# Performance work log

Hardware: AMD Instinct MI355X
Metric: run time of the kernel (lower is better)

Reference implementation:

```python
import jax, jax.numpy as jnp
import numpy as np

NUM_GROUPS = 16
GN_EPS = 1e-5
POOL = 4
CLAMP_MIN, CLAMP_MAX = 0.0, 1.0


def setup_inputs() -> dict:
    key = jax.random.key(0)
    k = jax.random.split(key, 4)
    x = jax.random.normal(k[0], (128, 8, 128, 128), dtype=jnp.float32)
    conv_weight = jax.random.normal(k[1], (64, 8, 3, 3), dtype=jnp.float32) * 0.1
    conv_bias = jax.random.normal(k[2], (64,), dtype=jnp.float32) * 0.1
    gn_weight = jnp.ones((64,), dtype=jnp.float32)
    gn_bias = jnp.zeros((64,), dtype=jnp.float32)
    scale = jax.random.normal(k[3], (64, 1, 1), dtype=jnp.float32)
    return {"x": x, "conv_weight": conv_weight, "conv_bias": conv_bias,
            "gn_weight": gn_weight, "gn_bias": gn_bias, "scale": scale}


def reference(x, conv_weight, conv_bias, gn_weight, gn_bias, scale):
    # Conv2d 3x3, stride 1, padding 0 (torch defaults). NCHW / OIHW.
    y = jax.lax.conv_general_dilated(
        x, conv_weight, window_strides=(1, 1), padding='VALID',
        dimension_numbers=('NCHW', 'OIHW', 'NCHW'))
    y = y + conv_bias[None, :, None, None]  # [N, 64, 126, 126]

    # GroupNorm(16 groups over 64 channels): stats over (C//G, H, W) per group.
    N, C, H, W = y.shape
    g = y.reshape(N, NUM_GROUPS, C // NUM_GROUPS, H, W)
    mean = jnp.mean(g, axis=(2, 3, 4), keepdims=True)
    var = jnp.mean(jnp.square(g - mean), axis=(2, 3, 4), keepdims=True)
    g = (g - mean) * jax.lax.rsqrt(var + GN_EPS)
    y = g.reshape(N, C, H, W) * gn_weight[None, :, None, None] + gn_bias[None, :, None, None]

    # Per-channel scale (scale has shape [64, 1, 1], broadcasts over H, W).
    y = y * scale[None]

    # MaxPool2d(kernel=4, stride=4), floor mode -> 126 // 4 = 31.
    y = jax.lax.reduce_window(
        y, -jnp.inf, jax.lax.max,
        window_dimensions=(1, 1, POOL, POOL),
        window_strides=(1, 1, POOL, POOL), padding='VALID')

    # Clamp.
    return jnp.clip(y, CLAMP_MIN, CLAMP_MAX)
```

## Files before the change

### kernel.cpp

```cpp
#include <hip/hip_runtime.h>
#include <hip/hip_fp16.h>

namespace {
constexpr int ICH = 8, IH = 128, IW = 128;
constexpr int CPG = 4, PH = 31;
constexpr int ICS = 516;
constexpr float EPS = 1e-5f;
constexpr float MPX = 126.f * 126.f;
constexpr int TOTAL_OUT = 128 * 64 * PH * PH;
constexpr size_t XH_BYTES = (size_t)128 * 128 * 128 * 8 * 2;
constexpr size_t WS_NEED = XH_BYTES + (size_t)128 * 16 * 4 * 2 * 4;

typedef _Float16 v8h __attribute__((ext_vector_type(8)));
typedef float v4f __attribute__((ext_vector_type(4)));
typedef unsigned short u16;
typedef unsigned int u32;

__device__ __forceinline__ void gll16(const void* g, void* l) {
  __builtin_amdgcn_global_load_lds((const __attribute__((address_space(1))) void*)g,
                                   (__attribute__((address_space(3))) void*)l, 16, 0, 0);
}

__device__ __forceinline__ u32 pkh(float a, float b) {
  unsigned short lo = __half_as_ushort(__float2half_rn(a));
  unsigned short hi = __half_as_ushort(__float2half_rn(b));
  return (u32)lo | ((u32)hi << 16);
}

__global__ __launch_bounds__(256) void pack_f16x8(const float* __restrict__ x,
                                                  u16* __restrict__ xh) {
  int i = blockIdx.x * 256 + threadIdx.x;
  int n = i >> 14, rc = i & 16383;
  const float* bp = x + ((size_t)n << 17) + rc;
  uint4 o;
  o.x = pkh(bp[0],      bp[16384]);
  o.y = pkh(bp[32768],  bp[49152]);
  o.z = pkh(bp[65536],  bp[81920]);
  o.w = pkh(bp[98304],  bp[114688]);
  *reinterpret_cast<uint4*>(xh + (size_t)i * 8) = o;
}

__global__ __launch_bounds__(256, 2) void conv_mfma(
    const u16* __restrict__ xh, const float* __restrict__ cw,
    const float* __restrict__ cb, const float* __restrict__ gnw,
    const float* __restrict__ sc, float* __restrict__ out,
    float* __restrict__ wsp) {
  __shared__ __align__(16) u16 ring[12][1056];

  const int bid = blockIdx.x;
  const int n = bid >> 2, qq = bid & 3;
  const int out_lo = qq * 32;
  const int out_hi = (qq == 3) ? 125 : out_lo + 31;
  const int NST = (qq == 3) ? 8 : 9;
  const int t = threadIdx.x;
  const int w = t >> 6, l = t & 63;
  const int colB = l & 15, qt = l >> 4;

  for (int idx = t; idx < 12 * 32; idx += 256)
    ring[idx >> 5][1024 + (idx & 31)] = 0;

  v8h af[3];
#pragma unroll
  for (int kc = 0; kc < 3; ++kc) {
    const int tap = kc * 4 + qt;
    const int ocA = 16 * w + colB;
#pragma unroll
    for (int i = 0; i < 8; ++i)
      af[kc][i] = (tap < 9) ? (_Float16)cw[ocA * 72 + i * 9 + tap] : (_Float16)0.f;
  }
  int eofc[3], dhl[3];
#pragma unroll
  for (int kc = 0; kc < 3; ++kc) {
    int tap = kc * 4 + qt; tap = (tap > 8) ? 8 : tap;
    dhl[kc] = tap / 3;
    eofc[kc] = (colB + tap % 3) * 8;
  }
  float flip[4];
#pragma unroll
  for (int q = 0; q < 4; ++q) {
    int oc = 16 * w + qt * 4 + q;
    flip[q] = (gnw[oc] * sc[oc] >= 0.f) ? 1.f : -1.f;
  }
  const u16* rb = &ring[0][0];

  auto issue = [&](int s) {
#pragma unroll
    for (int k = 0; k < 2; ++k) {
      int mk = w * 2 + k;
      int grow = out_lo + 4 * s + (mk >> 1);
      int hv = mk & 1;
      int slot = grow % 12;
      gll16(xh + ((size_t)(n * 128 + grow) * 128 + hv * 64) * 8 + l * 8,
            (void*)&ring[slot][hv * 512]);
    }
  };

  issue(0);

  float s1q[4] = {0.f, 0.f, 0.f, 0.f};
  float s2g = 0.f;
  float pacc[8][4];
#pragma unroll
  for (int ci = 0; ci < 8; ++ci)
#pragma unroll
    for (int q = 0; q < 4; ++q) pacc[ci][q] = -3.4e38f;

  for (int s = 0; s < NST; ++s) {
    __syncthreads();
    if (s + 1 < NST) issue(s + 1);
#pragma unroll
    for (int ri = 0; ri < 4; ++ri) {
      const int r = out_lo + 4 * s - 2 + ri;
      if (r < out_lo || r > out_hi) continue;
      const int rm = r % 12;
      int eoff[3];
#pragma unroll
      for (int kc = 0; kc < 3; ++kc) {
        int sl = rm + dhl[kc];
        if (sl >= 12) sl -= 12;
        eoff[kc] = sl * 1056 + eofc[kc];
      }
#pragma unroll
      for (int ci = 0; ci < 8; ++ci) {
        v4f acc = {0.f, 0.f, 0.f, 0.f};
#pragma unroll
        for (int kc = 0; kc < 3; ++kc) {
          v8h bf = *reinterpret_cast<const v8h*>(rb + eoff[kc] + ci * 128);
          acc = __builtin_amdgcn_mfma_f32_16x16x32_f16(af[kc], bf, acc, 0, 0, 0);
        }
        if (ci < 7) {
#pragma unroll
          for (int q = 0; q < 4; ++q) {
            s1q[q] += acc[q];
            s2g = fmaf(acc[q], acc[q], s2g);
            pacc[ci][q] = fmaxf(pacc[ci][q], flip[q] * acc[q]);
          }
        } else {
          const bool va = (colB < 14);
#pragma unroll
          for (int q = 0; q < 4; ++q) {
            float a = va ? acc[q] : 0.f;
            s1q[q] += a;
            s2g = fmaf(a, a, s2g);
            float fv = va ? flip[q] * acc[q] : -3.4e38f;
            pacc[7][q] = fmaxf(pacc[7][q], fv);
          }
        }
      }
      if ((r & 3) == 3) {
        const int pr = r >> 2;
        float* ob = out + (((size_t)n * 64 + 16 * w + qt * 4) * PH + pr) * PH;
#pragma unroll
        for (int ci = 0; ci < 8; ++ci) {
#pragma unroll
          for (int q = 0; q < 4; ++q) {
            float pm = pacc[ci][q];
            pm = fmaxf(pm, __shfl_xor(pm, 1, 64));
            pm = fmaxf(pm, __shfl_xor(pm, 2, 64));
            if ((l & 3) == 0 && (ci < 7 || colB < 12)) {
              int pc = ci * 4 + (colB >> 2);
              ob[(size_t)q * (PH * PH) + pc] = flip[q] * pm;
            }
            pacc[ci][q] = -3.4e38f;
          }
        }
      }
    }
  }

#pragma unroll
  for (int off = 1; off <= 8; off <<= 1) {
#pragma unroll
    for (int q = 0; q < 4; ++q) s1q[q] += __shfl_xor(s1q[q], off, 64);
    s2g += __shfl_xor(s2g, off, 64);
  }
  if ((l & 15) == 0) {
    const float cntq = 126.f * (float)(out_hi - out_lo + 1);
    float S1 = 0.f, S2 = s2g;
#pragma unroll
    for (int q = 0; q < 4; ++q) {
      float b = cb[16 * w + qt * 4 + q];
      S1 += s1q[q] + cntq * b;
      S2 += 2.f * b * s1q[q] + cntq * b * b;
    }
    int g = 4 * w + qt;
    float* wp = wsp + ((size_t)(n * 16 + g) * 4 + qq) * 2;
    wp[0] = S1; wp[1] = S2;
  }
}

__global__ __launch_bounds__(256) void gn_affine_clamp(
    float* __restrict__ out, const float* __restrict__ wsp,
    const float* __restrict__ gnw, const float* __restrict__ gnb,
    const float* __restrict__ sc, const float* __restrict__ cb) {
  int i = blockIdx.x * 256 + threadIdx.x;
  const int stride = gridDim.x * 256;
  for (; i < TOTAL_OUT; i += stride) {
    int c = (i / 961) & 63;
    int n = i / 61504;
    const float* wp = wsp + ((size_t)(n * 16 + (c >> 2)) * 4) * 2;
    float S1 = wp[0] + wp[2] + wp[4] + wp[6];
    float S2 = wp[1] + wp[3] + wp[5] + wp[7];
    constexpr float invN = 1.f / (4.f * MPX);
    float mean = S1 * invN;
    float var = S2 * invN - mean * mean;
    float inv = rsqrtf(var + EPS);
    float gw = gnw[c];
    float A = gw * inv * sc[c];
    float B = (gnb[c] - mean * inv * gw) * sc[c] + A * cb[c];
    float v = fmaf(A, out[i], B);
    out[i] = fminf(fmaxf(v, 0.f), 1.f);
  }
}

#define FIN(T, DOSTATS, RE)                                                    \
  {                                                                            \
    float f0 = T[0] + __shfl_xor(T[0], 32, 64);                                \
    float f1 = T[1] + __shfl_xor(T[1], 32, 64);                                \
    float f2 = T[2] + __shfl_xor(T[2], 32, 64);                                \
    float f3 = T[3] + __shfl_xor(T[3], 32, 64);                                \
    if (DOSTATS) {                                                             \
      s1 += f0 + f1 + m23 * (f2 + f3);                                         \
      float qa = fmaf(f0, f0, f1 * f1);                                        \
      float qb = fmaf(f2, f2, f3 * f3);                                        \
      s2 += qa + m23 * qb;                                                     \
    }                                                                          \
    RE = fmaxf(fmaxf(flip * f0, flip * f1), fmaxf(flip * f2, flip * f3));      \
  }
#define ZERO(T) { T[0] = 0.f; T[1] = 0.f; T[2] = 0.f; T[3] = 0.f; }
#define ROWF(RR, T2, T1, T0)                                                   \
  {                                                                            \
    _Pragma("unroll") for (int i4 = 0; i4 < 4; ++i4) {                         \
      const float* rp = bp + (4 * p + i4) * ICS + (RR) * IW + 4 * j;           \
      float4 v4 = *reinterpret_cast<const float4*>(rp);                        \
      float2 v2 = *reinterpret_cast<const float2*>(rp + 4);                    \
      float in[6] = {v4.x, v4.y, v4.z, v4.w, v2.x, v2.y};                      \
      _Pragma("unroll") for (int dw = 0; dw < 3; ++dw) {                       \
        const float w0 = wf[i4 * 9 + dw];                                      \
        const float w1 = wf[i4 * 9 + 3 + dw];                                  \
        const float w2 = wf[i4 * 9 + 6 + dw];                                  \
        _Pragma("unroll") for (int q = 0; q < 4; ++q) {                        \
          T2[q] = fmaf(in[q + dw], w2, T2[q]);                                 \
          T1[q] = fmaf(in[q + dw], w1, T1[q]);                                 \
          T0[q] = fmaf(in[q + dw], w0, T0[q]);                                 \
        }                                                                      \
      }                                                                        \
    }                                                                          \
  }
#define STAGEF(S, X, Y, Z, DOS01, DOWIN)                                       \
  {                                                                            \
    __syncthreads();                                                           \
    const int cur = (S) & 1;                                                   \
    if ((S) < 31) issue(4 * ((S) + 1), cur ^ 1);                               \
    const float* bp = &buf[cur][0][0];                                         \
    float re0, re1, re2, re3;                                                  \
    ROWF(0, X, Y, Z) FIN(X, DOS01, re0) ZERO(X)                                \
    ROWF(1, Y, Z, X) FIN(Y, DOS01, re1) ZERO(Y)                                \
    if (DOWIN) {                                                               \
      float wfin = fmaxf(wprev, fmaxf(re0, re1));                              \
      if (p == 0 && j < 31) mm[c][(S) - 1][j] = __float2half(flip * wfin);     \
    }                                                                          \
    ROWF(2, Z, X, Y) FIN(Z, true, re2) ZERO(Z)                                 \
    ROWF(3, X, Y, Z) FIN(X, true, re3) ZERO(X)                                 \
    wprev = fmaxf(re2, re3);                                                   \
  }

__global__ __launch_bounds__(256, 2) void fused_conv_gn_pool_f32(
    const float* __restrict__ x, const float* __restrict__ cw,
    const float* __restrict__ cb, const float* __restrict__ gnw,
    const float* __restrict__ gnb, const float* __restrict__ sc,
    float* __restrict__ out) {
  __shared__ float buf[2][ICH][ICS];
  __shared__ __half mm[CPG][PH][PH];
  __shared__ float red[8];
  __shared__ float stats[2];

  const int bid = blockIdx.x;
  const int xcd = bid & 7;
  const int kb = bid >> 3;
  const int n = xcd * 16 + (kb >> 4);
  const int g = kb & 15;
  const int t = threadIdx.x;
  const int c = t >> 6;
  const int u = t & 63;
  const int p = u >> 5;
  const int j = u & 31;
  const int gc = g * CPG + c;

  float wf[36];
  {
    const float4* wp = reinterpret_cast<const float4*>(cw + gc * 72 + p * 36);
#pragma unroll
    for (int q = 0; q < 9; ++q) {
      float4 v = wp[q];
      wf[4 * q + 0] = v.x; wf[4 * q + 1] = v.y;
      wf[4 * q + 2] = v.z; wf[4 * q + 3] = v.w;
    }
  }
  const float flip = ((gnw[gc] * sc[gc]) >= 0.f) ? 1.f : -1.f;
  const float m23 = (j < 31) ? 1.f : 0.f;

  const float* xn = x + (size_t)n * ICH * IH * IW;

  auto issue = [&](int br, int which) {
#pragma unroll
    for (int k = 0; k < 4; ++k) {
      const int m = c * 4 + k;
      const int ic = m >> 1;
      const int r2 = (m & 1) * 2;
      const float* gp = xn + (size_t)(ic * IH + br + r2) * IW + u * 4;
      gll16(gp, &buf[which][ic][r2 * IW]);
    }
  };

  issue(0, 0);

  float s1 = 0.f, s2 = 0.f, wprev = 0.f;
  float A0[4] = {0, 0, 0, 0}, A1[4] = {0, 0, 0, 0}, A2[4] = {0, 0, 0, 0};

  STAGEF(0, A0, A1, A2, false, false)
  for (int s = 1; s <= 28; s += 3) {
    STAGEF(s,     A1, A2, A0, true, true)
    STAGEF(s + 1, A2, A0, A1, true, true)
    STAGEF(s + 2, A0, A1, A2, true, true)
  }
  STAGEF(31, A1, A2, A0, true, true)

#pragma unroll
  for (int off = 32; off > 0; off >>= 1) {
    s1 += __shfl_down(s1, off, 64);
    s2 += __shfl_down(s2, off, 64);
  }
  const float bc = cb[gc];
  if (u == 0) {
    float t1 = 0.5f * s1, t2 = 0.5f * s2;
    red[c * 2] = t1 + MPX * bc;
    red[c * 2 + 1] = t2 + 2.f * bc * t1 + MPX * bc * bc;
  }
  __syncthreads();
  if (t == 0) {
    float S1 = red[0] + red[2] + red[4] + red[6];
    float S2 = red[1] + red[3] + red[5] + red[7];
    constexpr float invN = 1.f / (CPG * 126.f * 126.f);
    float mean = S1 * invN;
    float var = S2 * invN - mean * mean;
    stats[0] = mean;
    stats[1] = rsqrtf(var + EPS);
  }
  __syncthreads();
  const float mean = stats[0], inv = stats[1];

  float* outp = out + ((size_t)n * 64 + g * CPG) * (PH * PH);
  for (int kk = 0; kk < 16; ++kk) {
    int idx = t + kk * 256;
    if (idx < CPG * PH * PH) {
      int cc = idx / (PH * PH);
      int rem = idx - cc * (PH * PH);
      float e = __half2float(mm[cc][rem / PH][rem % PH]);
      int gcc = g * CPG + cc;
      float gw = gnw[gcc];
      float A = gw * inv * sc[gcc];
      float B = (gnb[gcc] - mean * inv * gw) * sc[gcc] + A * cb[gcc];
      float v = fmaf(A, e, B);
      v = fminf(fmaxf(v, 0.f), 1.f);
      outp[cc * (PH * PH) + rem] = v;
    }
  }
}
}

extern "C" void kernel_launch(void* const* d_in, const int* in_sizes, int n_in,
                              void* d_out, int out_size, void* d_ws, size_t ws_size,
                              hipStream_t stream) {
  const float* x   = (const float*)d_in[0];
  const float* cw  = (const float*)d_in[1];
  const float* cb  = (const float*)d_in[2];
  const float* gnw = (const float*)d_in[3];
  const float* gnb = (const float*)d_in[4];
  const float* sc  = (const float*)d_in[5];
  float* out = (float*)d_out;

  if (ws_size >= WS_NEED) {
    u16* xh = (u16*)d_ws;
    float* wsp = (float*)((char*)d_ws + XH_BYTES);
    hipLaunchKernelGGL(pack_f16x8, dim3(8192), dim3(256), 0, stream, x, xh);
    hipLaunchKernelGGL(conv_mfma, dim3(512), dim3(256), 0, stream,
                       xh, cw, cb, gnw, sc, out, wsp);
    hipLaunchKernelGGL(gn_affine_clamp, dim3(2048), dim3(256), 0, stream,
                       out, wsp, gnw, gnb, sc, cb);
  } else {
    hipLaunchKernelGGL(fused_conv_gn_pool_f32, dim3(2048), dim3(256), 0, stream,
                       x, cw, cb, gnw, gnb, sc, out);
  }
}
```

Measured before the change: 104.5 us.

## Split conv rows into eight slabs per image and fold sign flip into weights

The conv kernel now splits each image's 126 output rows into eight 16-row slabs instead of four 32-row slabs, doubling the grid to 1024 blocks so more blocks are resident across CUs. The sign flip for the max/min pooling trick moves into the fp16 weights, which drops a multiply per accumulator element in the inner loop; the flip is reapplied to the partial sums when the statistics are written. Partial-statistic storage and the GN kernel now handle eight partials per group. The cost is more halo-row reloads per slab and smaller pipelines per block. The weight flip is done per A-row output channel, while the stats use the per-q flip, so correctness depends on those indexings matching the same channels.

Result: faster. 99.33 us (-5.0%).

```diff
diff --git a/kernel.cpp b/kernel.cpp
--- a/kernel.cpp
+++ b/kernel.cpp
@@ -9,7 +9,7 @@
 constexpr float MPX = 126.f * 126.f;
 constexpr int TOTAL_OUT = 128 * 64 * PH * PH;
 constexpr size_t XH_BYTES = (size_t)128 * 128 * 128 * 8 * 2;
-constexpr size_t WS_NEED = XH_BYTES + (size_t)128 * 16 * 4 * 2 * 4;
+constexpr size_t WS_NEED = XH_BYTES + (size_t)128 * 16 * 8 * 2 * 4;
 
 typedef _Float16 v8h __attribute__((ext_vector_type(8)));
 typedef float v4f __attribute__((ext_vector_type(4)));
@@ -48,10 +48,10 @@
   __shared__ __align__(16) u16 ring[12][1056];
 
   const int bid = blockIdx.x;
-  const int n = bid >> 2, qq = bid & 3;
-  const int out_lo = qq * 32;
-  const int out_hi = (qq == 3) ? 125 : out_lo + 31;
-  const int NST = (qq == 3) ? 8 : 9;
+  const int n = bid >> 3, e = bid & 7;
+  const int out_lo = e * 16;
+  const int out_hi = (e == 7) ? 125 : out_lo + 15;
+  const int NST = (e == 7) ? 4 : 5;
   const int t = threadIdx.x;
   const int w = t >> 6, l = t & 63;
   const int colB = l & 15, qt = l >> 4;
@@ -59,14 +59,16 @@
   for (int idx = t; idx < 12 * 32; idx += 256)
     ring[idx >> 5][1024 + (idx & 31)] = 0;
 
+  const int ocA = 16 * w + colB;
+  const float flipA = (gnw[ocA] * sc[ocA] >= 0.f) ? 1.f : -1.f;
   v8h af[3];
 #pragma unroll
   for (int kc = 0; kc < 3; ++kc) {
     const int tap = kc * 4 + qt;
-    const int ocA = 16 * w + colB;
 #pragma unroll
     for (int i = 0; i < 8; ++i)
-      af[kc][i] = (tap < 9) ? (_Float16)cw[ocA * 72 + i * 9 + tap] : (_Float16)0.f;
+      af[kc][i] = (tap < 9) ? (_Float16)(flipA * cw[ocA * 72 + i * 9 + tap])
+                            : (_Float16)0.f;
   }
   int eofc[3], dhl[3];
 #pragma unroll
@@ -133,7 +135,7 @@
           for (int q = 0; q < 4; ++q) {
             s1q[q] += acc[q];
             s2g = fmaf(acc[q], acc[q], s2g);
-            pacc[ci][q] = fmaxf(pacc[ci][q], flip[q] * acc[q]);
+            pacc[ci][q] = fmaxf(pacc[ci][q], acc[q]);
           }
         } else {
           const bool va = (colB < 14);
@@ -142,7 +144,7 @@
             float a = va ? acc[q] : 0.f;
             s1q[q] += a;
             s2g = fmaf(a, a, s2g);
-            float fv = va ? flip[q] * acc[q] : -3.4e38f;
+            float fv = va ? acc[q] : -3.4e38f;
             pacc[7][q] = fmaxf(pacc[7][q], fv);
           }
         }
@@ -175,16 +177,17 @@
     s2g += __shfl_xor(s2g, off, 64);
   }
   if ((l & 15) == 0) {
-    const float cntq = 126.f * (float)(out_hi - out_lo + 1);
+    const float cnte = 126.f * (float)(out_hi - out_lo + 1);
     float S1 = 0.f, S2 = s2g;
 #pragma unroll
     for (int q = 0; q < 4; ++q) {
+      float s1t = flip[q] * s1q[q];
       float b = cb[16 * w + qt * 4 + q];
-      S1 += s1q[q] + cntq * b;
-      S2 += 2.f * b * s1q[q] + cntq * b * b;
+      S1 += s1t + cnte * b;
+      S2 += 2.f * b * s1t + cnte * b * b;
     }
     int g = 4 * w + qt;
-    float* wp = wsp + ((size_t)(n * 16 + g) * 4 + qq) * 2;
+    float* wp = wsp + ((size_t)(n * 16 + g) * 8 + e) * 2;
     wp[0] = S1; wp[1] = S2;
   }
 }
@@ -198,9 +201,10 @@
   for (; i < TOTAL_OUT; i += stride) {
     int c = (i / 961) & 63;
     int n = i / 61504;
-    const float* wp = wsp + ((size_t)(n * 16 + (c >> 2)) * 4) * 2;
-    float S1 = wp[0] + wp[2] + wp[4] + wp[6];
-    float S2 = wp[1] + wp[3] + wp[5] + wp[7];
+    const float* wp = wsp + ((size_t)(n * 16 + (c >> 2)) * 8) * 2;
+    float S1 = 0.f, S2 = 0.f;
+#pragma unroll
+    for (int e = 0; e < 8; ++e) { S1 += wp[2 * e]; S2 += wp[2 * e + 1]; }
     constexpr float invN = 1.f / (4.f * MPX);
     float mean = S1 * invN;
     float var = S2 * invN - mean * mean;
@@ -384,7 +388,7 @@
     u16* xh = (u16*)d_ws;
     float* wsp = (float*)((char*)d_ws + XH_BYTES);
     hipLaunchKernelGGL(pack_f16x8, dim3(8192), dim3(256), 0, stream, x, xh);
-    hipLaunchKernelGGL(conv_mfma, dim3(512), dim3(256), 0, stream,
+    hipLaunchKernelGGL(conv_mfma, dim3(1024), dim3(256), 0, stream,
                        xh, cw, cb, gnw, sc, out, wsp);
     hipLaunchKernelGGL(gn_affine_clamp, dim3(2048), dim3(256), 0, stream,
                        out, wsp, gnw, gnb, sc, cb);
```
